# Kernel optimization log

Measured on AMD Instinct MI355X. Metric: run time of the kernel, lower is better.

## Reference

```python
import jax, jax.numpy as jnp
import numpy as np

N = 100000   # number of website nodes
E = 800000   # edges per edge type
F = 128      # in_feats == out_feats
NEG_SLOPE = 0.2


def setup_inputs() -> dict:
    key = jax.random.key(0)
    ks = jax.random.split(key, 16)
    s = 1.0 / np.sqrt(F)
    return {
        "feat": jax.random.normal(ks[0], (N, F), jnp.float32),
        "src_u": jax.random.randint(ks[1], (E,), 0, N),
        "dst_u": jax.random.randint(ks[2], (E,), 0, N),
        "src_r": jax.random.randint(ks[3], (E,), 0, N),
        "dst_r": jax.random.randint(ks[4], (E,), 0, N),
        # fc_self (no bias)
        "W_self": jax.random.uniform(ks[5], (F, F), jnp.float32, -s, s),
        # attn branch 'user'
        "W_u": jax.random.uniform(ks[6], (F, F), jnp.float32, -s, s),
        "a_l_u": jax.random.uniform(ks[7], (F,), jnp.float32, -s, s),
        "a_r_u": jax.random.uniform(ks[8], (F,), jnp.float32, -s, s),
        # attn branch 'reuse'
        "W_r": jax.random.uniform(ks[9], (F, F), jnp.float32, -s, s),
        "a_l_r": jax.random.uniform(ks[10], (F,), jnp.float32, -s, s),
        "a_r_r": jax.random.uniform(ks[11], (F,), jnp.float32, -s, s),
        # fc_neigh (with bias)
        "W_neigh": jax.random.uniform(ks[12], (F, F), jnp.float32, -s, s),
        "b_neigh": jax.random.uniform(ks[13], (F,), jnp.float32, -s, s),
        # module-level bias parameter
        "bias": jnp.zeros((F,), jnp.float32),
    }


def _attn_aggregate(feat, W, a_l, a_r, src, dst, n_nodes):
    """GAT-style single-head aggregation over one edge type.
    Returns [n_nodes, F] = sum_{e: dst(e)=v} softmax_v(leaky_relu(el[src]+er[dst])) * h[src]."""
    h = feat @ W                                    # [N, F] (feat_src == feat_dst)
    el = h @ a_l                                    # [N]
    er = h @ a_r                                    # [N]
    e = jax.nn.leaky_relu(el[src] + er[dst], NEG_SLOPE)   # [E]
    # edge_softmax: normalize over incoming edges of each dst node
    m = jax.ops.segment_max(e, dst, num_segments=n_nodes)  # [N] (-inf for isolated dst, unused)
    ex = jnp.exp(e - m[dst])                        # [E]
    denom = jax.ops.segment_sum(ex, dst, num_segments=n_nodes)  # [N]
    a = ex / denom[dst]                             # [E]
    msg = h[src] * a[:, None]                       # [E, F]
    return jax.ops.segment_sum(msg, dst, num_segments=n_nodes)  # [N, F]


def reference(feat, src_u, dst_u, src_r, dst_r, W_self, W_u, a_l_u, a_r_u,
              W_r, a_l_r, a_r_r, W_neigh, b_neigh, bias):
    n = feat.shape[0]
    neigh_u = _attn_aggregate(feat, W_u, a_l_u, a_r_u, src_u, dst_u, n)
    neigh_r = _attn_aggregate(feat, W_r, a_l_r, a_r_r, src_r, dst_r, n)
    # multi_update_all cross reducer 'mean' over the two edge types
    neigh = 0.5 * (neigh_u + neigh_r)
    h_neigh = neigh @ W_neigh + b_neigh             # fc_neigh
    rst = feat @ W_self + h_neigh                   # fc_self(h_self) + h_neigh
    return rst + bias
```

## Files before the change

kernel.cpp:

```cpp
#include <hip/hip_runtime.h>

#define F 128
#define NEG_SLOPE 0.2f
#define SHIFT 9
#define BPB 512
#define NBS 512

typedef _Float16 f16_t;
typedef _Float16 f16x8 __attribute__((ext_vector_type(8)));
typedef _Float16 f16x2 __attribute__((ext_vector_type(2)));
typedef float f32x4 __attribute__((ext_vector_type(4)));

__global__ __launch_bounds__(128) void prep_mats(
    const float* __restrict__ Wu, const float* __restrict__ Wr,
    const float* __restrict__ Ws, const float* __restrict__ Wn,
    const float* __restrict__ alu, const float* __restrict__ aru,
    const float* __restrict__ alr, const float* __restrict__ arr_,
    f16_t* __restrict__ Mtu, f16_t* __restrict__ Mtr, f16_t* __restrict__ Wts,
    float* __restrict__ wlu, float* __restrict__ wru,
    float* __restrict__ wlr, float* __restrict__ wrr)
{
    int b = blockIdx.x;
    int tid = threadIdx.x;
    if (b < 256) {
        int k = b & 127;
        const float* W = (b < 128) ? Wu : Wr;
        f16_t* M = (b < 128) ? Mtu : Mtr;
        float acc = 0.f;
        for (int t = 0; t < F; t++) acc += W[k * F + t] * Wn[t * F + tid];
        M[tid * F + k] = (f16_t)acc;
    } else if (b < 384) {
        int c = b - 256;
        Wts[c * F + tid] = (f16_t)Ws[tid * F + c];
    } else {
        int which = b - 384;
        const float* W = (which < 2) ? Wu : Wr;
        const float* a = (which == 0) ? alu : (which == 1) ? aru : (which == 2) ? alr : arr_;
        float acc = 0.f;
        for (int c = 0; c < F; c++) acc += W[tid * F + c] * a[c];
        float* o = (which == 0) ? wlu : (which == 1) ? wru : (which == 2) ? wlr : wrr;
        o[tid] = acc;
    }
}


__global__ __launch_bounds__(256) void cast_p1a(
    const float* __restrict__ feat,
    const float* __restrict__ wlu, const float* __restrict__ wru,
    const float* __restrict__ wlr, const float* __restrict__ wrr,
    f16_t* __restrict__ featb,
    float* __restrict__ elu, float* __restrict__ eru,
    float* __restrict__ elr, float* __restrict__ err_,
    const int* __restrict__ dst_u, const int* __restrict__ dst_r,
    int* __restrict__ cnt_bb,
    int Eu, int Et, int N, int chunk, int n, int nbk)
{
    int b = blockIdx.x;
    int tid = threadIdx.x;
    if (b < 256) {
        __shared__ int hist[NBS];
        for (int i = tid; i < NBS; i += 256) hist[i] = 0;
        __syncthreads();
        int e0 = b * chunk;
        int e1 = e0 + chunk; if (e1 > Et) e1 = Et;
        int u1 = (e1 < Eu) ? e1 : Eu;
        for (int e = e0 + tid; e < u1; e += 256) {
            int bin = dst_u[e];
            atomicAdd(&hist[bin >> SHIFT], 1);
        }
        int r0 = (e0 > Eu) ? e0 : Eu;
        for (int e = r0 + tid; e < e1; e += 256) {
            int bin = N + dst_r[e - Eu];
            atomicAdd(&hist[bin >> SHIFT], 1);
        }
        __syncthreads();
        for (int i = tid; i < NBS; i += 256) cnt_bb[b * NBS + i] = hist[i];
        return;
    }
    int fid = b - 256;
    int lane = tid & 63;
    int wave = tid >> 6;
    int lo = lane & 15, hi = lane >> 4;
    int base = fid * 64 + wave * 16;
    if (base >= n) return;
    int row = base + lo;
    if (row > n - 1) row = n - 1;
    const float* fp = feat + (size_t)row * F + hi * 8;
    f16_t* fb = featb + (size_t)row * F + hi * 8;
    const float* wsel = (lo == 0) ? wlu : (lo == 1) ? wru : (lo == 2) ? wlr : wrr;

    f32x4 acc = (f32x4){0.f, 0.f, 0.f, 0.f};
#pragma unroll
    for (int ks = 0; ks < 4; ks++) {
        float4 a0 = *(const float4*)(fp + ks * 32);
        float4 a1 = *(const float4*)(fp + ks * 32 + 4);
        f16x8 af;
        af[0] = (f16_t)a0.x; af[1] = (f16_t)a0.y; af[2] = (f16_t)a0.z; af[3] = (f16_t)a0.w;
        af[4] = (f16_t)a1.x; af[5] = (f16_t)a1.y; af[6] = (f16_t)a1.z; af[7] = (f16_t)a1.w;
        *(f16x8*)(fb + ks * 32) = af;
        f16x8 bf;
#pragma unroll
        for (int q = 0; q < 8; q++) bf[q] = (f16_t)0;
        if (lo < 4) {
            float4 b0 = *(const float4*)(wsel + ks * 32 + hi * 8);
            float4 b1 = *(const float4*)(wsel + ks * 32 + hi * 8 + 4);
            bf[0] = (f16_t)b0.x; bf[1] = (f16_t)b0.y; bf[2] = (f16_t)b0.z; bf[3] = (f16_t)b0.w;
            bf[4] = (f16_t)b1.x; bf[5] = (f16_t)b1.y; bf[6] = (f16_t)b1.z; bf[7] = (f16_t)b1.w;
        }
        acc = __builtin_amdgcn_mfma_f32_16x16x32_f16(af, bf, acc, 0, 0, 0);
    }
    if (lo < 4) {
        float* oarr = (lo == 0) ? elu : (lo == 1) ? eru : (lo == 2) ? elr : err_;
#pragma unroll
        for (int j = 0; j < 4; j++) {
            int r = base + hi * 4 + j;
            if (r < n) oarr[r] = acc[j];
        }
    }
}


__global__ __launch_bounds__(256) void scan_bb1(int* __restrict__ cnt_bb,
                                                int* __restrict__ btot, int nbk)
{
    int k = blockIdx.x;
    int tid = threadIdx.x;
    __shared__ int lds[256];
    int v = cnt_bb[tid * NBS + k];
    lds[tid] = v;
    __syncthreads();
    for (int off = 1; off < 256; off <<= 1) {
        int add = (tid >= off) ? lds[tid - off] : 0;
        __syncthreads();
        lds[tid] += add;
        __syncthreads();
    }
    cnt_bb[tid * NBS + k] = lds[tid] - v;
    if (tid == 255) btot[k] = lds[255];
}

__global__ __launch_bounds__(512) void scan_bb2(const int* __restrict__ btot,
                                                int* __restrict__ bbase,
                                                int* __restrict__ rp,
                                                int nbk, int twoN, int Et)
{
    __shared__ int lds[512];
    int t = threadIdx.x;
    int v = (t < nbk) ? btot[t] : 0;
    lds[t] = v;
    __syncthreads();
    for (int off = 1; off < 512; off <<= 1) {
        int add = (t >= off) ? lds[t - off] : 0;
        __syncthreads();
        lds[t] += add;
        __syncthreads();
    }
    bbase[t] = lds[t] - v;
    if (t == 0) rp[twoN] = Et;
}


__global__ __launch_bounds__(256) void p1b_scatter(
    const int* __restrict__ src_u, const int* __restrict__ dst_u,
    const int* __restrict__ src_r, const int* __restrict__ dst_r,
    const int* __restrict__ cnt_bb, const int* __restrict__ bbase,
    unsigned* __restrict__ bucketed,
    int Eu, int Et, int N, int chunk, int nbk)
{
    int b = blockIdx.x;
    int tid = threadIdx.x;
    __shared__ int cur[NBS];
    for (int i = tid; i < nbk; i += 256) cur[i] = bbase[i] + cnt_bb[b * NBS + i];
    __syncthreads();
    int e0 = b * chunk;
    int e1 = e0 + chunk; if (e1 > Et) e1 = Et;
    int u1 = (e1 < Eu) ? e1 : Eu;
    for (int e = e0 + tid; e < u1; e += 256) {
        int bin = dst_u[e];
        int s = src_u[e];
        int pos = atomicAdd(&cur[bin >> SHIFT], 1);
        bucketed[pos] = (unsigned)s | ((unsigned)(bin & (BPB - 1)) << 17);
    }
    int r0 = (e0 > Eu) ? e0 : Eu;
    for (int e = r0 + tid; e < e1; e += 256) {
        int bin = N + dst_r[e - Eu];
        int s = src_r[e - Eu];
        int pos = atomicAdd(&cur[bin >> SHIFT], 1);
        bucketed[pos] = (unsigned)s | ((unsigned)(bin & (BPB - 1)) << 17);
    }
}


__global__ __launch_bounds__(512) void p2_build(
    const unsigned* __restrict__ bucketed, const int* __restrict__ bbase,
    int* __restrict__ rp, int* __restrict__ csr, int twoN)
{
    int k = blockIdx.x;
    int tid = threadIdx.x;
    int beg = bbase[k], end = bbase[k + 1];
    __shared__ int hist[BPB];
    __shared__ int psum[512];
    hist[tid] = 0;
    __syncthreads();
    for (int i = beg + tid; i < end; i += 512) {
        unsigned w = bucketed[i];
        atomicAdd(&hist[(w >> 17) & (BPB - 1)], 1);
    }
    __syncthreads();
    int v = hist[tid];
    psum[tid] = v;
    __syncthreads();
    for (int off = 1; off < 512; off <<= 1) {
        int add = (tid >= off) ? psum[tid - off] : 0;
        __syncthreads();
        psum[tid] += add;
        __syncthreads();
    }
    int base = beg + psum[tid] - v;
    int bin = (k << SHIFT) + tid;
    if (bin < twoN) rp[bin] = base;
    hist[tid] = base;
    __syncthreads();
    for (int i = beg + tid; i < end; i += 512) {
        unsigned w = bucketed[i];
        int src = (int)(w & 0x1FFFF);
        int pos = atomicAdd(&hist[(w >> 17) & (BPB - 1)], 1);
        csr[pos] = src;
    }
}


__global__ __launch_bounds__(256) void aggregate_v4(
    const f16_t* __restrict__ featb,
    const float* __restrict__ elu, const float* __restrict__ eru,
    const float* __restrict__ elr, const float* __restrict__ err_,
    const int* __restrict__ rp, const int* __restrict__ csr,
    f16_t* __restrict__ aggu, f16_t* __restrict__ aggr, int n)
{
    int wave = (int)(((size_t)blockIdx.x * 256 + threadIdx.x) >> 6);
    int lane = threadIdx.x & 63;
    int g = lane >> 4, lo = lane & 15;
    int dst = wave * 4 + g;
    bool alive = (dst < n);
    int dc = alive ? dst : (n - 1);

    int iu = rp[dc], endu = rp[dc + 1];
    int ir = rp[n + dc], endr = rp[n + dc + 1];
    if (!alive) { endu = iu; endr = ir; }
    float ervu = eru[dc];
    float ervr = err_[dc];

    union UV { f16x8 v; f16x2 p[4]; };
    f16x2 z = {(f16_t)0, (f16_t)0};
    f16x2 au0 = z, au1 = z, au2 = z, au3 = z;
    f16x2 ar0 = z, ar1 = z, ar2 = z, ar3 = z;
    float du = 0.f, dr = 0.f;

    bool vu0 = iu     < endu, vu1 = iu + 1 < endu;
    bool vr0 = ir     < endr, vr1 = ir + 1 < endr;
    int cu0 = csr[vu0 ? iu     : 0];
    int cu1 = csr[vu1 ? iu + 1 : 0];
    int cr0 = csr[vr0 ? ir     : 0];
    int cr1 = csr[vr1 ? ir + 1 : 0];
    UV hu0, hu1, hr0, hr1;
    hu0.v = *(const f16x8*)&featb[(size_t)cu0 * F + lo * 8];
    hu1.v = *(const f16x8*)&featb[(size_t)cu1 * F + lo * 8];
    hr0.v = *(const f16x8*)&featb[(size_t)cr0 * F + lo * 8];
    hr1.v = *(const f16x8*)&featb[(size_t)cr1 * F + lo * 8];

    while (iu < endu || ir < endr) {
        int ju = iu + 2, jr = ir + 2;
        bool nvu0 = ju     < endu, nvu1 = ju + 1 < endu;
        bool nvr0 = jr     < endr, nvr1 = jr + 1 < endr;
        int ncu0 = csr[nvu0 ? ju     : 0];
        int ncu1 = csr[nvu1 ? ju + 1 : 0];
        int ncr0 = csr[nvr0 ? jr     : 0];
        int ncr1 = csr[nvr1 ? jr + 1 : 0];
        UV pu0, pu1, pr0, pr1;
        pu0.v = *(const f16x8*)&featb[(size_t)ncu0 * F + lo * 8];
        pu1.v = *(const f16x8*)&featb[(size_t)ncu1 * F + lo * 8];
        pr0.v = *(const f16x8*)&featb[(size_t)ncr0 * F + lo * 8];
        pr1.v = *(const f16x8*)&featb[(size_t)ncr1 * F + lo * 8];

        {
            float e = elu[cu0] + ervu; e = fmaxf(e, NEG_SLOPE * e);
            float ex = vu0 ? __expf(e) : 0.f;
            f16_t w = (f16_t)ex; f16x2 wv = {w, w};
            au0 += wv * hu0.p[0]; au1 += wv * hu0.p[1];
            au2 += wv * hu0.p[2]; au3 += wv * hu0.p[3];
            du += ex;
        }
        {
            float e = elu[cu1] + ervu; e = fmaxf(e, NEG_SLOPE * e);
            float ex = vu1 ? __expf(e) : 0.f;
            f16_t w = (f16_t)ex; f16x2 wv = {w, w};
            au0 += wv * hu1.p[0]; au1 += wv * hu1.p[1];
            au2 += wv * hu1.p[2]; au3 += wv * hu1.p[3];
            du += ex;
        }
        {
            float e = elr[cr0] + ervr; e = fmaxf(e, NEG_SLOPE * e);
            float ex = vr0 ? __expf(e) : 0.f;
            f16_t w = (f16_t)ex; f16x2 wv = {w, w};
            ar0 += wv * hr0.p[0]; ar1 += wv * hr0.p[1];
            ar2 += wv * hr0.p[2]; ar3 += wv * hr0.p[3];
            dr += ex;
        }
        {
            float e = elr[cr1] + ervr; e = fmaxf(e, NEG_SLOPE * e);
            float ex = vr1 ? __expf(e) : 0.f;
            f16_t w = (f16_t)ex; f16x2 wv = {w, w};
            ar0 += wv * hr1.p[0]; ar1 += wv * hr1.p[1];
            ar2 += wv * hr1.p[2]; ar3 += wv * hr1.p[3];
            dr += ex;
        }

        hu0 = pu0; hu1 = pu1; hr0 = pr0; hr1 = pr1;
        cu0 = ncu0; cu1 = ncu1; cr0 = ncr0; cr1 = ncr1;
        vu0 = nvu0; vu1 = nvu1; vr0 = nvr0; vr1 = nvr1;
        iu = ju; ir = jr;
    }

    if (alive) {
        float invu = (du > 0.f) ? 0.5f / du : 0.f;
        float invr = (dr > 0.f) ? 0.5f / dr : 0.f;
        f16_t ihu = (f16_t)invu, ihr = (f16_t)invr;
        f16x2 ivu = {ihu, ihu}, ivr = {ihr, ihr};
        UV ou, orr;
        ou.p[0] = au0 * ivu; ou.p[1] = au1 * ivu; ou.p[2] = au2 * ivu; ou.p[3] = au3 * ivu;
        orr.p[0] = ar0 * ivr; orr.p[1] = ar1 * ivr; orr.p[2] = ar2 * ivr; orr.p[3] = ar3 * ivr;
        *(f16x8*)&aggu[(size_t)dst * F + lo * 8] = ou.v;
        *(f16x8*)&aggr[(size_t)dst * F + lo * 8] = orr.v;
    }
}


__global__ __launch_bounds__(1024) void mfma_final3(
    const f16_t* __restrict__ featb,
    const f16_t* __restrict__ aggu, const f16_t* __restrict__ aggr,
    const f16_t* __restrict__ Wts, const f16_t* __restrict__ Mtu,
    const f16_t* __restrict__ Mtr,
    const float* __restrict__ bn, const float* __restrict__ bias,
    float* __restrict__ out, int n, int ntiles)
{
    __shared__ f16_t Ls[F * F];
    __shared__ f16_t Lu[F * F];
    __shared__ f16_t Lr[F * F];
    for (int i = threadIdx.x; i < 2048; i += 1024) {
        int c = i >> 4, kc = i & 15, kcs = kc ^ (c & 15);
        *(f16x8*)&Ls[c * F + kcs * 8] = *(const f16x8*)&Wts[c * F + kc * 8];
        *(f16x8*)&Lu[c * F + kcs * 8] = *(const f16x8*)&Mtu[c * F + kc * 8];
        *(f16x8*)&Lr[c * F + kcs * 8] = *(const f16x8*)&Mtr[c * F + kc * 8];
    }
    __syncthreads();

    int lane = threadIdx.x & 63;
    int wave = threadIdx.x >> 6;
    int lo = lane & 15, hi = lane >> 4;

    float cb[8];
#pragma unroll
    for (int t = 0; t < 8; t++) cb[t] = bn[t * 16 + lo] + bias[t * 16 + lo];

    for (int tile = blockIdx.x; tile < ntiles; tile += 256) {
        int row0 = tile * 256 + wave * 16;
        if (row0 >= n) continue;
        int arow = row0 + lo;
        if (arow > n - 1) arow = n - 1;
        const f16_t* pf = featb + (size_t)arow * F + hi * 8;
        const f16_t* pu = aggu + (size_t)arow * F + hi * 8;
        const f16_t* pr = aggr + (size_t)arow * F + hi * 8;

        f32x4 acc[8];
#pragma unroll
        for (int t = 0; t < 8; t++) acc[t] = (f32x4){0.f, 0.f, 0.f, 0.f};

#pragma unroll
        for (int ks = 0; ks < 4; ks++) {
            f16x8 a1 = *(const f16x8*)(pf + ks * 32);
            f16x8 a2 = *(const f16x8*)(pu + ks * 32);
            f16x8 a3 = *(const f16x8*)(pr + ks * 32);
#pragma unroll
            for (int t = 0; t < 8; t++) {
                int c = t * 16 + lo;
                int kcs = (ks * 4 + hi) ^ lo;
                f16x8 bs = *(const f16x8*)&Ls[c * F + kcs * 8];
                f16x8 bu = *(const f16x8*)&Lu[c * F + kcs * 8];
                f16x8 br = *(const f16x8*)&Lr[c * F + kcs * 8];
                acc[t] = __builtin_amdgcn_mfma_f32_16x16x32_f16(a1, bs, acc[t], 0, 0, 0);
                acc[t] = __builtin_amdgcn_mfma_f32_16x16x32_f16(a2, bu, acc[t], 0, 0, 0);
                acc[t] = __builtin_amdgcn_mfma_f32_16x16x32_f16(a3, br, acc[t], 0, 0, 0);
            }
        }

#pragma unroll
        for (int j = 0; j < 4; j++) {
            int r = row0 + hi * 4 + j;
            if (r < n) {
                float* op = out + (size_t)r * F + lo;
#pragma unroll
                for (int t = 0; t < 8; t++) op[t * 16] = acc[t][j] + cb[t];
            }
        }
    }
}


extern "C" void kernel_launch(void* const* d_in, const int* in_sizes, int n_in,
                              void* d_out, int out_size, void* d_ws, size_t ws_size,
                              hipStream_t stream) {
    const float* feat   = (const float*)d_in[0];
    const int*   src_u  = (const int*)d_in[1];
    const int*   dst_u  = (const int*)d_in[2];
    const int*   src_r  = (const int*)d_in[3];
    const int*   dst_r  = (const int*)d_in[4];
    const float* W_self = (const float*)d_in[5];
    const float* W_u    = (const float*)d_in[6];
    const float* a_l_u  = (const float*)d_in[7];
    const float* a_r_u  = (const float*)d_in[8];
    const float* W_r    = (const float*)d_in[9];
    const float* a_l_r  = (const float*)d_in[10];
    const float* a_r_r  = (const float*)d_in[11];
    const float* W_ngh  = (const float*)d_in[12];
    const float* b_ngh  = (const float*)d_in[13];
    const float* bias   = (const float*)d_in[14];
    float* out = (float*)d_out;

    const int N  = in_sizes[0] / F;
    const int Eu = in_sizes[1];
    const int Er = in_sizes[3];
    const int Et = Eu + Er;
    const int twoN = 2 * N;
    const int nbk = (twoN + BPB - 1) >> SHIFT;

    char* ws = (char*)d_ws;
    size_t off = 0;
    auto alloc = [&](size_t bytes) -> void* {
        void* p = ws + off;
        off = (off + bytes + 255) & ~(size_t)255;
        return p;
    };
    f16_t* featb = (f16_t*)alloc((size_t)N * F * 2);
    f16_t* aggu  = (f16_t*)alloc((size_t)N * F * 2);
    f16_t* aggr  = (f16_t*)alloc((size_t)N * F * 2);
    f16_t* Mt_u  = (f16_t*)alloc((size_t)F * F * 2);
    f16_t* Mt_r  = (f16_t*)alloc((size_t)F * F * 2);
    f16_t* Wt_s  = (f16_t*)alloc((size_t)F * F * 2);
    float* wlu = (float*)alloc((size_t)F * 4);
    float* wru = (float*)alloc((size_t)F * 4);
    float* wlr = (float*)alloc((size_t)F * 4);
    float* wrr = (float*)alloc((size_t)F * 4);
    float* elu = (float*)alloc((size_t)N * 4);
    float* eru = (float*)alloc((size_t)N * 4);
    float* elr = (float*)alloc((size_t)N * 4);
    float* err_ = (float*)alloc((size_t)N * 4);
    int* cnt_bb = (int*)alloc((size_t)256 * NBS * 4);
    int* btot   = (int*)alloc((size_t)NBS * 4);
    int* bbase  = (int*)alloc((size_t)(NBS + 1) * 4);
    int* rp2    = (int*)alloc(((size_t)twoN + 1) * 4);
    unsigned* bucketed = (unsigned*)alloc((size_t)Et * 4);
    int* csr2   = (int*)alloc((size_t)Et * 4);

    prep_mats<<<388, 128, 0, stream>>>(W_u, W_r, W_self, W_ngh,
                                       a_l_u, a_r_u, a_l_r, a_r_r,
                                       Mt_u, Mt_r, Wt_s, wlu, wru, wlr, wrr);

    const int chunk = (Et + 255) / 256;
    int castBlocks = (N + 63) / 64;
    cast_p1a<<<256 + castBlocks, 256, 0, stream>>>(
        feat, wlu, wru, wlr, wrr, featb, elu, eru, elr, err_,
        dst_u, dst_r, cnt_bb, Eu, Et, N, chunk, N, nbk);

    scan_bb1<<<nbk, 256, 0, stream>>>(cnt_bb, btot, nbk);
    scan_bb2<<<1, 512, 0, stream>>>(btot, bbase, rp2, nbk, twoN, Et);
    p1b_scatter<<<256, 256, 0, stream>>>(src_u, dst_u, src_r, dst_r,
                                         cnt_bb, bbase, bucketed,
                                         Eu, Et, N, chunk, nbk);
    p2_build<<<nbk, 512, 0, stream>>>(bucketed, bbase, rp2, csr2, twoN);

    aggregate_v4<<<(N + 15) / 16, 256, 0, stream>>>(featb, elu, eru, elr, err_,
                                                    rp2, csr2, aggu, aggr, N);
    int ntiles = (N + 255) / 256;
    mfma_final3<<<256, 1024, 0, stream>>>(featb, aggu, aggr,
                                          Wt_s, Mt_u, Mt_r,
                                          b_ngh, bias, out, N, ntiles);
}
```

Baseline: 150.7 us.

## Fuse attention aggregation with final MFMA projection via shared-memory tiles

Merges the aggregation kernel and the final MFMA GEMM kernel into one. Each 256-thread block aggregates 16 destination rows into swizzled shared memory, then its four waves each compute two 16-column output tiles by reading the weight matrices straight from global memory. This drops the fp16 aggu/aggr round trip through HBM and one kernel launch. In exchange, every block re-reads all three 128x128 weight matrices from global or cache instead of staging them once in LDS, and the GEMM is split into small per-block pieces.

```diff
diff --git a/kernel.cpp b/kernel.cpp
--- a/kernel.cpp
+++ b/kernel.cpp
@@ -230,17 +230,25 @@
 }
 
 
-__global__ __launch_bounds__(256) void aggregate_v4(
+__global__ __launch_bounds__(256) void aggregate_final2(
     const f16_t* __restrict__ featb,
     const float* __restrict__ elu, const float* __restrict__ eru,
     const float* __restrict__ elr, const float* __restrict__ err_,
     const int* __restrict__ rp, const int* __restrict__ csr,
-    f16_t* __restrict__ aggu, f16_t* __restrict__ aggr, int n)
-{
-    int wave = (int)(((size_t)blockIdx.x * 256 + threadIdx.x) >> 6);
-    int lane = threadIdx.x & 63;
+    const f16_t* __restrict__ Wts, const f16_t* __restrict__ Mtu,
+    const f16_t* __restrict__ Mtr,
+    const float* __restrict__ bn, const float* __restrict__ bias,
+    float* __restrict__ out, int n)
+{
+    __shared__ f16_t Au[16 * F];
+    __shared__ f16_t Ar[16 * F];
+    int tid = threadIdx.x;
+    int lane = tid & 63;
+    int wavIn = tid >> 6;
     int g = lane >> 4, lo = lane & 15;
-    int dst = wave * 4 + g;
+    int blk0 = blockIdx.x * 16;
+    int d16 = wavIn * 4 + g;
+    int dst = blk0 + d16;
     bool alive = (dst < n);
     int dc = alive ? dst : (n - 1);
 
@@ -321,7 +329,7 @@
         iu = ju; ir = jr;
     }
 
-    if (alive) {
+    {
         float invu = (du > 0.f) ? 0.5f / du : 0.f;
         float invr = (dr > 0.f) ? 0.5f / dr : 0.f;
         f16_t ihu = (f16_t)invu, ihr = (f16_t)invr;
@@ -329,78 +337,53 @@
         UV ou, orr;
         ou.p[0] = au0 * ivu; ou.p[1] = au1 * ivu; ou.p[2] = au2 * ivu; ou.p[3] = au3 * ivu;
         orr.p[0] = ar0 * ivr; orr.p[1] = ar1 * ivr; orr.p[2] = ar2 * ivr; orr.p[3] = ar3 * ivr;
-        *(f16x8*)&aggu[(size_t)dst * F + lo * 8] = ou.v;
-        *(f16x8*)&aggr[(size_t)dst * F + lo * 8] = orr.v;
-    }
-}
-
-
-__global__ __launch_bounds__(1024) void mfma_final3(
-    const f16_t* __restrict__ featb,
-    const f16_t* __restrict__ aggu, const f16_t* __restrict__ aggr,
-    const f16_t* __restrict__ Wts, const f16_t* __restrict__ Mtu,
-    const f16_t* __restrict__ Mtr,
-    const float* __restrict__ bn, const float* __restrict__ bias,
-    float* __restrict__ out, int n, int ntiles)
-{
-    __shared__ f16_t Ls[F * F];
-    __shared__ f16_t Lu[F * F];
-    __shared__ f16_t Lr[F * F];
-    for (int i = threadIdx.x; i < 2048; i += 1024) {
-        int c = i >> 4, kc = i & 15, kcs = kc ^ (c & 15);
-        *(f16x8*)&Ls[c * F + kcs * 8] = *(const f16x8*)&Wts[c * F + kc * 8];
-        *(f16x8*)&Lu[c * F + kcs * 8] = *(const f16x8*)&Mtu[c * F + kc * 8];
-        *(f16x8*)&Lr[c * F + kcs * 8] = *(const f16x8*)&Mtr[c * F + kc * 8];
-    }
-    __syncthreads();
-
-    int lane = threadIdx.x & 63;
-    int wave = threadIdx.x >> 6;
-    int lo = lane & 15, hi = lane >> 4;
-
-    float cb[8];
+        int sb = ((lo ^ d16) & 15) * 8;
+        *(f16x8*)&Au[d16 * F + sb] = ou.v;
+        *(f16x8*)&Ar[d16 * F + sb] = orr.v;
+    }
+    __syncthreads();
+
+    int lo2 = lo, hi2 = g;
+    int t0 = wavIn * 2;
+    float cb0 = bn[t0 * 16 + lo2]      + bias[t0 * 16 + lo2];
+    float cb1 = bn[(t0 + 1) * 16 + lo2] + bias[(t0 + 1) * 16 + lo2];
+    int arow = blk0 + lo2;
+    if (arow > n - 1) arow = n - 1;
+    const f16_t* pf = featb + (size_t)arow * F + hi2 * 8;
+    int c0 = t0 * 16 + lo2;
+    int c1 = c0 + 16;
+
+    f32x4 acc0 = (f32x4){0.f, 0.f, 0.f, 0.f};
+    f32x4 acc1 = (f32x4){0.f, 0.f, 0.f, 0.f};
 #pragma unroll
-    for (int t = 0; t < 8; t++) cb[t] = bn[t * 16 + lo] + bias[t * 16 + lo];
-
-    for (int tile = blockIdx.x; tile < ntiles; tile += 256) {
-        int row0 = tile * 256 + wave * 16;
-        if (row0 >= n) continue;
-        int arow = row0 + lo;
-        if (arow > n - 1) arow = n - 1;
-        const f16_t* pf = featb + (size_t)arow * F + hi * 8;
-        const f16_t* pu = aggu + (size_t)arow * F + hi * 8;
-        const f16_t* pr = aggr + (size_t)arow * F + hi * 8;
-
-        f32x4 acc[8];
+    for (int ks = 0; ks < 4; ks++) {
+        f16x8 a1 = *(const f16x8*)(pf + ks * 32);
+        int kc = ks * 4 + hi2;
+        int kcs = (kc ^ lo2) & 15;
+        f16x8 a2 = *(const f16x8*)&Au[lo2 * F + kcs * 8];
+        f16x8 a3 = *(const f16x8*)&Ar[lo2 * F + kcs * 8];
+        int ko = ks * 32 + hi2 * 8;
+        f16x8 bs0 = *(const f16x8*)&Wts[c0 * F + ko];
+        f16x8 bu0 = *(const f16x8*)&Mtu[c0 * F + ko];
+        f16x8 br0 = *(const f16x8*)&Mtr[c0 * F + ko];
+        acc0 = __builtin_amdgcn_mfma_f32_16x16x32_f16(a1, bs0, acc0, 0, 0, 0);
+        acc0 = __builtin_amdgcn_mfma_f32_16x16x32_f16(a2, bu0, acc0, 0, 0, 0);
+        acc0 = __builtin_amdgcn_mfma_f32_16x16x32_f16(a3, br0, acc0, 0, 0, 0);
+        f16x8 bs1 = *(const f16x8*)&Wts[c1 * F + ko];
+        f16x8 bu1 = *(const f16x8*)&Mtu[c1 * F + ko];
+        f16x8 br1 = *(const f16x8*)&Mtr[c1 * F + ko];
+        acc1 = __builtin_amdgcn_mfma_f32_16x16x32_f16(a1, bs1, acc1, 0, 0, 0);
+        acc1 = __builtin_amdgcn_mfma_f32_16x16x32_f16(a2, bu1, acc1, 0, 0, 0);
+        acc1 = __builtin_amdgcn_mfma_f32_16x16x32_f16(a3, br1, acc1, 0, 0, 0);
+    }
+
 #pragma unroll
-        for (int t = 0; t < 8; t++) acc[t] = (f32x4){0.f, 0.f, 0.f, 0.f};
-
-#pragma unroll
-        for (int ks = 0; ks < 4; ks++) {
-            f16x8 a1 = *(const f16x8*)(pf + ks * 32);
-            f16x8 a2 = *(const f16x8*)(pu + ks * 32);
-            f16x8 a3 = *(const f16x8*)(pr + ks * 32);
-#pragma unroll
-            for (int t = 0; t < 8; t++) {
-                int c = t * 16 + lo;
-                int kcs = (ks * 4 + hi) ^ lo;
-                f16x8 bs = *(const f16x8*)&Ls[c * F + kcs * 8];
-                f16x8 bu = *(const f16x8*)&Lu[c * F + kcs * 8];
-                f16x8 br = *(const f16x8*)&Lr[c * F + kcs * 8];
-                acc[t] = __builtin_amdgcn_mfma_f32_16x16x32_f16(a1, bs, acc[t], 0, 0, 0);
-                acc[t] = __builtin_amdgcn_mfma_f32_16x16x32_f16(a2, bu, acc[t], 0, 0, 0);
-                acc[t] = __builtin_amdgcn_mfma_f32_16x16x32_f16(a3, br, acc[t], 0, 0, 0);
-            }
-        }
-
-#pragma unroll
-        for (int j = 0; j < 4; j++) {
-            int r = row0 + hi * 4 + j;
-            if (r < n) {
-                float* op = out + (size_t)r * F + lo;
-#pragma unroll
-                for (int t = 0; t < 8; t++) op[t * 16] = acc[t][j] + cb[t];
-            }
+    for (int j = 0; j < 4; j++) {
+        int r = blk0 + hi2 * 4 + j;
+        if (r < n) {
+            float* op = out + (size_t)r * F;
+            op[t0 * 16 + lo2]       = acc0[j] + cb0;
+            op[(t0 + 1) * 16 + lo2] = acc1[j] + cb1;
         }
     }
 }
@@ -441,8 +424,6 @@
         return p;
     };
     f16_t* featb = (f16_t*)alloc((size_t)N * F * 2);
-    f16_t* aggu  = (f16_t*)alloc((size_t)N * F * 2);
-    f16_t* aggr  = (f16_t*)alloc((size_t)N * F * 2);
     f16_t* Mt_u  = (f16_t*)alloc((size_t)F * F * 2);
     f16_t* Mt_r  = (f16_t*)alloc((size_t)F * F * 2);
     f16_t* Wt_s  = (f16_t*)alloc((size_t)F * F * 2);
@@ -478,10 +459,8 @@
                                          Eu, Et, N, chunk, nbk);
     p2_build<<<nbk, 512, 0, stream>>>(bucketed, bbase, rp2, csr2, twoN);
 
-    aggregate_v4<<<(N + 15) / 16, 256, 0, stream>>>(featb, elu, eru, elr, err_,
-                                                    rp2, csr2, aggu, aggr, N);
-    int ntiles = (N + 255) / 256;
-    mfma_final3<<<256, 1024, 0, stream>>>(featb, aggu, aggr,
-                                          Wt_s, Mt_u, Mt_r,
-                                          b_ngh, bias, out, N, ntiles);
-}
+    int nblk = (N + 15) / 16;
+    aggregate_final2<<<nblk, 256, 0, stream>>>(featb, elu, eru, elr, err_,
+                                               rp2, csr2, Wt_s, Mt_u, Mt_r,
+                                               b_ngh, bias, out, N);
+}
```

After: 184.2 us. +22.3%, slower.
